# Optimization experiments

Hardware: AMD Instinct MI355X
Metric: run time of the kernel (lower is better)

Reference implementation:

```python
import jax, jax.numpy as jnp
import numpy as np

B, P, D = 32, 2048, 256  # batch, patch_num, input_dim


def setup_inputs() -> dict:
    key = jax.random.key(0)
    ks = jax.random.split(key, 6)
    n = lambda k, shape: jax.random.normal(k, shape, dtype=jnp.float32) * 0.02
    return {
        "x": jax.random.normal(ks[0], (B, P, D), dtype=jnp.float32),
        "mlp_w": n(ks[1], (D, D)), "mlp_b": jnp.zeros((D,), jnp.float32),
        "his_w": n(ks[2], (D, D)), "his_b": jnp.zeros((D,), jnp.float32),
        "cur_w": n(ks[3], (D, D)), "cur_b": jnp.zeros((D,), jnp.float32),
        "wl_w": n(ks[4], (D, P)), "wl_b": jnp.zeros((P,), jnp.float32),
        "gate_w": n(ks[5], (D, 1)), "gate_b": jnp.zeros((1,), jnp.float32),
        "ln_g": jnp.ones((D,), jnp.float32), "ln_b": jnp.zeros((D,), jnp.float32),
    }


def _layernorm(h, g, b, eps=1e-5):
    mu = h.mean(-1, keepdims=True)
    var = ((h - mu) ** 2).mean(-1, keepdims=True)
    return (h - mu) * jax.lax.rsqrt(var + eps) * g + b


def reference(x, mlp_w, mlp_b, his_w, his_b, cur_w, cur_b, wl_w, wl_b,
              gate_w, gate_b, ln_g, ln_b):
    origin = x
    # expert_num == 0 -> MoE branch skipped, x unchanged
    H = origin @ his_w + his_b                              # extractor_his: [B,P,D]
    # gate(extractor_cur(origin)) -> [B,P,1], repeated along last dim == broadcast
    weight_current = (origin @ cur_w + cur_b) @ gate_w + gate_b  # [B,P,1]
    logits = H @ wl_w + wl_b                                # [B,P,P]
    weight = jax.nn.softmax(logits, axis=-1)                # row softmax
    adj = jnp.tril(weight)                                  # causal mask (diagonal=0)
    aggregated = jnp.einsum('bpq,bqd->bpd', adj, origin)    # [B,P,D]
    H_history = aggregated @ mlp_w + mlp_b                  # dropout is identity (p=0)
    H_current = weight_current * origin
    out = _layernorm(H_history + H_current, ln_g, ln_b)     # aggregated_norm == 1
    return (out, origin)
```

## Files before the change

kernel.cpp:

```cpp
#include <hip/hip_runtime.h>
#include <hip/hip_bf16.h>

typedef __attribute__((ext_vector_type(8))) short s8v;
typedef __attribute__((ext_vector_type(4))) float f4v;
typedef __attribute__((ext_vector_type(4))) unsigned int u4v;

#define BATCH 32
#define SEQ   2048
#define DIM   256
#define ORIGIN_OFF ((size_t)BATCH * SEQ * DIM)

#define XT_OFF  0ull
#define WL_OFF  16777216ull
#define HIS_OFF 17301504ull
#define MLP_OFF 17367040ull

#define OFF_A 0
#define OFF_B 33792
#define OFF_C 79872
#define XT_LDS 9216

__device__ __forceinline__ unsigned short f2bf(float f) {
  __hip_bfloat16 h = __float2bfloat16(f);
  return *reinterpret_cast<unsigned short*>(&h);
}
__device__ __forceinline__ f4v mfma16(s8v a, s8v b, f4v c) {
  return __builtin_amdgcn_mfma_f32_16x16x32_bf16(a, b, c, 0, 0, 0);
}
__device__ __forceinline__ unsigned int pk2(float lo, float hi) {
  return (unsigned int)f2bf(lo) | ((unsigned int)f2bf(hi) << 16);
}
__device__ __forceinline__ void dma16(const void* g, void* l) {
  __builtin_amdgcn_global_load_lds(
      (const __attribute__((address_space(1))) unsigned int*)g,
      (__attribute__((address_space(3))) unsigned int*)l, 16, 0, 0);
}


__global__ __launch_bounds__(256) void prep_w(
    const float* __restrict__ wl_w, const float* __restrict__ his_w,
    const float* __restrict__ mlp_w, unsigned short* __restrict__ ws)
{
  const int gid = blockIdx.x * 256 + threadIdx.x;
  const int row = gid >> 5;
  const int c0 = (gid & 31) * 8;
  const float* src; unsigned short* dst; int ld;
  if (row < 2048)      { src = wl_w + row;           ld = 2048; dst = ws + WL_OFF  + (size_t)row * 256 + c0; }
  else if (row < 2304) { src = his_w + (row - 2048); ld = 256;  dst = ws + HIS_OFF + (size_t)(row - 2048) * 256 + c0; }
  else                 { src = mlp_w + (row - 2304); ld = 256;  dst = ws + MLP_OFF + (size_t)(row - 2304) * 256 + c0; }
  u4v o;
  #pragma unroll
  for (int j = 0; j < 4; ++j) {
    const unsigned short lo = f2bf(src[(size_t)(c0 + 2 * j) * ld]);
    const unsigned short hi = f2bf(src[(size_t)(c0 + 2 * j + 1) * ld]);
    o[j] = (unsigned int)lo | ((unsigned int)hi << 16);
  }
  *(u4v*)dst = o;
}

__global__ __launch_bounds__(256) void prep_xt(
    const float* __restrict__ x, unsigned short* __restrict__ xT)
{
  __shared__ unsigned short tile[64][68];
  const int b = blockIdx.z, p0 = blockIdx.x * 64, d0 = blockIdx.y * 64;
  const int t = threadIdx.x;
  {
    const int r = t >> 2, c0 = (t & 3) * 16;
    const float* src = x + ((size_t)b * SEQ + p0 + r) * DIM + d0 + c0;
    #pragma unroll
    for (int j = 0; j < 4; ++j) {
      f4v v = *(const f4v*)(src + j * 4);
      tile[r][c0 + j * 4 + 0] = f2bf(v[0]);
      tile[r][c0 + j * 4 + 1] = f2bf(v[1]);
      tile[r][c0 + j * 4 + 2] = f2bf(v[2]);
      tile[r][c0 + j * 4 + 3] = f2bf(v[3]);
    }
  }
  __syncthreads();
  {
    const int dl = t >> 2, s0 = (t & 3) * 16;
    u4v o0, o1;
    #pragma unroll
    for (int j = 0; j < 4; ++j) {
      o0[j] = (unsigned int)tile[s0 + 2 * j][dl]     | ((unsigned int)tile[s0 + 2 * j + 1][dl] << 16);
      o1[j] = (unsigned int)tile[s0 + 8 + 2 * j][dl] | ((unsigned int)tile[s0 + 9 + 2 * j][dl] << 16);
    }
    unsigned short* dst = xT + ((size_t)b * DIM + d0 + dl) * SEQ + p0 + s0;
    *(u4v*)dst = o0;
    *(u4v*)(dst + 8) = o1;
  }
}


__device__ __forceinline__ void gemm_regA(
    const unsigned short* __restrict__ Wt,
    const s8v (&af)[2][8], f4v (&acc)[2][8],
    char* smem_, int tid, int col16, int quad, int wc, int x7, int wq)
{
  char* sB = smem_ + OFF_B;
  char* ldsW = sB + wq * 1024;
  const int wrow = tid >> 5;
  const int wu = (tid & 31) ^ wrow;
  for (int st = 0; st < 4; ++st) {
    if (st) __syncthreads();
    const unsigned short* src = Wt + (size_t)(st * 64 + wrow) * 256 + wu * 8;
    #pragma unroll
    for (int j = 0; j < 8; ++j) dma16(src + (size_t)j * 2048, ldsW + j * 4096);
    __syncthreads();
    #pragma unroll
    for (int s = 0; s < 8; ++s) {
      const int sl = (((s * 4 + quad) ^ x7) << 4);
      #pragma unroll
      for (int nt = 0; nt < 2; ++nt) {
        s8v bfr = *(const s8v*)(sB + (wc * 32 + nt * 16 + col16) * 512 + sl);
        acc[0][st * 2 + nt] = mfma16(af[0][s], bfr, acc[0][st * 2 + nt]);
        acc[1][st * 2 + nt] = mfma16(af[1][s], bfr, acc[1][st * 2 + nt]);
      }
    }
  }
}

__global__ __launch_bounds__(256, 2)
void tfs_kernel(
    const float* __restrict__ x,
    const float* __restrict__ mlp_b,
    const float* __restrict__ his_b,
    const float* __restrict__ cur_w,
    const float* __restrict__ cur_b,
    const float* __restrict__ wl_b,
    const float* __restrict__ gate_w,
    const float* __restrict__ gate_b,
    const float* __restrict__ ln_g,
    const float* __restrict__ ln_b,
    const unsigned short* __restrict__ wsp,
    float* __restrict__ out)
{
  __shared__ __align__(16) char smem[81408];
  char* sA = smem + OFF_A;
  char* sB = smem + OFF_B;
  char* sC = smem + OFF_C;

  const int tid = threadIdx.x;
  const int lane = tid & 63;
  const int col16 = lane & 15;
  const int quad = lane >> 4;
  const int w = tid >> 6;
  const int wr = w & 1, wc = w >> 1;
  const int rw = wr * 32;
  const int x7 = col16 & 7;
  const int wq = __builtin_amdgcn_readfirstlane(w);

  const int b = blockIdx.y;
  const int pidx = (blockIdx.x + ((blockIdx.y >> 3) & 3) * 8) & 31;
  const int p0 = pidx * 64;

  const float* xb = x + (size_t)b * SEQ * DIM;
  const unsigned short* wlT  = wsp + WL_OFF;
  const unsigned short* hisT = wsp + HIS_OFF;
  const unsigned short* mlpT = wsp + MLP_OFF;
  const unsigned short* xTb  = wsp + XT_OFF + (size_t)b * DIM * SEQ;
  const f4v zero4 = {0.f, 0.f, 0.f, 0.f};

  const int krow = tid >> 5;
  const int ku   = (tid & 31) ^ krow;
  const int xrow = tid >> 3;
  const int xu   = (tid & 7) ^ (xrow & 7);
  char* ldsK = smem + OFF_A + wq * 1024;
  char* ldsX = smem + OFF_B + XT_LDS + wq * 1024;

  s8v xf[2][8];
  #pragma unroll
  for (int a = 0; a < 2; ++a) {
    const int row = rw + a * 16 + col16;
    const float* srcx = xb + (size_t)(p0 + row) * DIM;
    #pragma unroll
    for (int s = 0; s < 8; ++s) {
      const int k0 = (s * 4 + quad) * 8;
      f4v v0 = *(const f4v*)(srcx + k0);
      f4v v1 = *(const f4v*)(srcx + k0 + 4);
      u4v o;
      o[0] = pk2(v0[0], v0[1]); o[1] = pk2(v0[2], v0[3]);
      o[2] = pk2(v1[0], v1[1]); o[3] = pk2(v1[2], v1[3]);
      xf[a][s] = *(s8v*)&o;
    }
  }

  f4v accQ[2][8];
  #pragma unroll
  for (int a = 0; a < 2; ++a)
    #pragma unroll
    for (int i = 0; i < 8; ++i) accQ[a][i] = zero4;
  gemm_regA(hisT, xf, accQ, smem, tid, col16, quad, wc, x7, wq);
  #pragma unroll
  for (int a = 0; a < 2; ++a)
    #pragma unroll
    for (int i = 0; i < 8; ++i) {
      const int n = (i >> 1) * 64 + wc * 32 + (i & 1) * 16 + col16;
      const float bias = his_b[n];
      #pragma unroll
      for (int r = 0; r < 4; ++r) {
        const int row = rw + a * 16 + quad * 4 + r;
        *(unsigned short*)(sA + row * 528 + n * 2) = f2bf(accQ[a][i][r] + bias);
      }
    }
  __syncthreads();
  s8v qf[2][8];
  #pragma unroll
  for (int a = 0; a < 2; ++a) {
    const int row = rw + a * 16 + col16;
    #pragma unroll
    for (int s = 0; s < 8; ++s)
      qf[a][s] = *(const s8v*)(sA + row * 528 + (s * 4 + quad) * 16);
  }
  __syncthreads();
  {
    const unsigned short* srck = wlT + (size_t)krow * 256 + ku * 8;
    #pragma unroll
    for (int j = 0; j < 8; ++j) dma16(srck + (size_t)j * 2048, ldsK + j * 4096);
  }
  __syncthreads();

  f4v accO[2][8];
  #pragma unroll
  for (int a = 0; a < 2; ++a)
    #pragma unroll
    for (int dt = 0; dt < 8; ++dt) accO[a][dt] = zero4;
  float mrun[2][4], Zrun[2][4], mrunT[2];
  #pragma unroll
  for (int a = 0; a < 2; ++a) {
    mrunT[a] = -1.0e30f;
    #pragma unroll
    for (int r = 0; r < 4; ++r) { mrun[a][r] = -1.0e30f; Zrun[a][r] = 0.f; }
  }
  float* stat_max = (float*)(sC);
  float* stat_sum = (float*)(sC + 512);
  char* sX = sB + XT_LDS;
  const int rk0 = (wc * 32 + col16) * 512;
  const int rk1 = rk0 + 16 * 512;

  #pragma unroll 1
  for (int qi = 0; qi < 32; ++qi) {
    const int q0 = qi * 64;
    const bool active = (q0 <= p0);

    f4v accST[2][2];
    accST[0][0] = zero4; accST[0][1] = zero4;
    accST[1][0] = zero4; accST[1][1] = zero4;
    #pragma unroll
    for (int s = 0; s < 8; ++s) {
      const int sl = (((s * 4 + quad) ^ x7) << 4);
      s8v kf0 = *(const s8v*)(sA + rk0 + sl);
      s8v kf1 = *(const s8v*)(sA + rk1 + sl);
      accST[0][0] = mfma16(kf0, qf[0][s], accST[0][0]);
      accST[0][1] = mfma16(kf0, qf[1][s], accST[0][1]);
      accST[1][0] = mfma16(kf1, qf[0][s], accST[1][0]);
      accST[1][1] = mfma16(kf1, qf[1][s], accST[1][1]);
    }
    #pragma unroll
    for (int t = 0; t < 2; ++t) {
      const f4v wb = *(const f4v*)(wl_b + q0 + wc * 32 + t * 16 + quad * 4);
      #pragma unroll
      for (int a = 0; a < 2; ++a)
        #pragma unroll
        for (int r = 0; r < 4; ++r) accST[t][a][r] += wb[r];
    }
    #pragma unroll
    for (int a = 0; a < 2; ++a) {
      float m = fmaxf(fmaxf(fmaxf(accST[0][a][0], accST[0][a][1]),
                            fmaxf(accST[0][a][2], accST[0][a][3])),
                      fmaxf(fmaxf(accST[1][a][0], accST[1][a][1]),
                            fmaxf(accST[1][a][2], accST[1][a][3])));
      m = fmaxf(m, __shfl_xor(m, 16, 64));
      m = fmaxf(m, __shfl_xor(m, 32, 64));
      if (quad == 0) stat_max[wc * 64 + rw + a * 16 + col16] = m;
    }
    __syncthreads();

    if (qi < 31) {
      const unsigned short* srck = wlT + (size_t)(q0 + 64 + krow) * 256 + ku * 8;
      #pragma unroll
      for (int j = 0; j < 8; ++j) dma16(srck + (size_t)j * 2048, ldsK + j * 4096);
    }
    if (active) {
      const unsigned short* srcx = xTb + (size_t)xrow * 2048 + q0 + xu * 8;
      #pragma unroll
      for (int j = 0; j < 8; ++j) dma16(srcx + (size_t)j * 65536, ldsX + j * 4096);
    }

    float alpha[2][4];
    #pragma unroll
    for (int a = 0; a < 2; ++a)
      #pragma unroll
      for (int r = 0; r < 4; ++r) {
        const int row = rw + a * 16 + quad * 4 + r;
        const float mt = fmaxf(stat_max[row], stat_max[64 + row]);
        const float mn = fmaxf(mrun[a][r], mt);
        alpha[a][r] = __expf(fminf(mrun[a][r] - mn, 0.f));
        mrun[a][r] = mn;
      }
    #pragma unroll
    for (int a = 0; a < 2; ++a) {
      const int p = rw + a * 16 + col16;
      mrunT[a] = fmaxf(mrunT[a], fmaxf(stat_max[p], stat_max[64 + p]));
    }
    float Pv[2][2][4];
    #pragma unroll
    for (int t = 0; t < 2; ++t)
      #pragma unroll
      for (int a = 0; a < 2; ++a)
        #pragma unroll
        for (int r = 0; r < 4; ++r)
          Pv[t][a][r] = __expf(fminf(accST[t][a][r] - mrunT[a], 0.f));
    #pragma unroll
    for (int a = 0; a < 2; ++a) {
      float s = ((Pv[0][a][0] + Pv[0][a][1]) + (Pv[0][a][2] + Pv[0][a][3]))
              + ((Pv[1][a][0] + Pv[1][a][1]) + (Pv[1][a][2] + Pv[1][a][3]));
      s += __shfl_xor(s, 16, 64);
      s += __shfl_xor(s, 32, 64);
      if (quad == 0) stat_sum[wc * 64 + rw + a * 16 + col16] = s;
    }
    if (active) {
      #pragma unroll
      for (int t = 0; t < 2; ++t)
        #pragma unroll
        for (int a = 0; a < 2; ++a) {
          const int p = rw + a * 16 + col16;
          #pragma unroll
          for (int r = 0; r < 4; ++r) {
            const int ql = wc * 32 + t * 16 + quad * 4 + r;
            const float pv = ((q0 + ql) <= (p0 + p)) ? Pv[t][a][r] : 0.f;
            *(unsigned short*)(sB + p * 144 + ql * 2) = f2bf(pv);
          }
        }
    }
    __syncthreads();

    #pragma unroll
    for (int a = 0; a < 2; ++a)
      #pragma unroll
      for (int r = 0; r < 4; ++r) {
        const int row = rw + a * 16 + quad * 4 + r;
        const float st = stat_sum[row] + stat_sum[64 + row];
        Zrun[a][r] = Zrun[a][r] * alpha[a][r] + st;
      }
    #pragma unroll
    for (int a = 0; a < 2; ++a)
      #pragma unroll
      for (int dt = 0; dt < 8; ++dt)
        #pragma unroll
        for (int r = 0; r < 4; ++r) accO[a][dt][r] *= alpha[a][r];

    if (active) {
      #pragma unroll
      for (int h = 0; h < 2; ++h) {
        s8v ap0 = *(const s8v*)(sB + (rw + col16) * 144 + (h * 4 + quad) * 16);
        s8v ap1 = *(const s8v*)(sB + (rw + 16 + col16) * 144 + (h * 4 + quad) * 16);
        const int slx = (((h * 4 + quad) ^ x7) << 4);
        #pragma unroll
        for (int dt = 0; dt < 8; ++dt) {
          const int d = wc * 128 + dt * 16 + col16;
          s8v bv = *(const s8v*)(sX + d * 128 + slx);
          accO[0][dt] = mfma16(ap0, bv, accO[0][dt]);
          accO[1][dt] = mfma16(ap1, bv, accO[1][dt]);
        }
      }
    }
  }

  #pragma unroll
  for (int a = 0; a < 2; ++a)
    #pragma unroll
    for (int dt = 0; dt < 8; ++dt) {
      const int d = wc * 128 + dt * 16 + col16;
      #pragma unroll
      for (int r = 0; r < 4; ++r) {
        const int row = rw + a * 16 + quad * 4 + r;
        const float invZ = 1.0f / fmaxf(Zrun[a][r], 1e-30f);
        *(unsigned short*)(sA + row * 528 + d * 2) = f2bf(accO[a][dt][r] * invZ);
      }
    }
  __syncthreads();
  s8v af[2][8];
  #pragma unroll
  for (int a = 0; a < 2; ++a) {
    const int row = rw + a * 16 + col16;
    #pragma unroll
    for (int s = 0; s < 8; ++s)
      af[a][s] = *(const s8v*)(sA + row * 528 + (s * 4 + quad) * 16);
  }
  f4v accH[2][8];
  #pragma unroll
  for (int a = 0; a < 2; ++a)
    #pragma unroll
    for (int i = 0; i < 8; ++i) accH[a][i] = zero4;
  gemm_regA(mlpT, af, accH, smem, tid, col16, quad, wc, x7, wq);
  __syncthreads();

  float* cgL = (float*)(sB + 24576);
  float* cbL = (float*)(sB + 25600);
  {
    const float* cw = cur_w + (size_t)tid * DIM;
    float s = 0.f;
    #pragma unroll 8
    for (int i = 0; i < 64; ++i) {
      f4v vc = *(const f4v*)(cw + i * 4);
      f4v vg = *(const f4v*)(gate_w + i * 4);
      s += vc[0] * vg[0] + vc[1] * vg[1] + vc[2] * vg[2] + vc[3] * vg[3];
    }
    cgL[tid] = s;
    if (tid == 0) {
      float s2 = 0.f;
      for (int j = 0; j < DIM; ++j) s2 += cur_b[j] * gate_w[j];
      cbL[0] = s2 + gate_b[0];
    }
  }
  __syncthreads();

  float* wp = (float*)sC;
  {
    const int row = tid & 63, sg = tid >> 6;
    const float* xr = xb + (size_t)(p0 + row) * DIM + sg * 64;
    const float* cgp = cgL + sg * 64;
    float sacc = 0.f;
    #pragma unroll
    for (int i = 0; i < 16; ++i) {
      f4v xv4 = *(const f4v*)(xr + i * 4);
      sacc += xv4[0] * cgp[i * 4] + xv4[1] * cgp[i * 4 + 1]
            + xv4[2] * cgp[i * 4 + 2] + xv4[3] * cgp[i * 4 + 3];
    }
    wp[row * 4 + sg] = sacc;
  }
  __syncthreads();
  float* wcS = (float*)sC;
  if (tid < 64) {
    const float v = wp[tid * 4] + wp[tid * 4 + 1] + wp[tid * 4 + 2] + wp[tid * 4 + 3] + cbL[0];
    wcS[tid] = v;
  }
  __syncthreads();

  float s1l[2][4], s2l[2][4];
  #pragma unroll
  for (int a = 0; a < 2; ++a)
    #pragma unroll
    for (int r = 0; r < 4; ++r) { s1l[a][r] = 0.f; s2l[a][r] = 0.f; }
  #pragma unroll
  for (int a = 0; a < 2; ++a)
    #pragma unroll
    for (int i = 0; i < 8; ++i) {
      const int n = (i >> 1) * 64 + wc * 32 + (i & 1) * 16 + col16;
      const float mb = mlp_b[n];
      #pragma unroll
      for (int r = 0; r < 4; ++r) {
        const int row = rw + a * 16 + quad * 4 + r;
        const float xv = xb[(size_t)(p0 + row) * DIM + n];
        const float v = accH[a][i][r] + mb + wcS[row] * xv;
        accH[a][i][r] = v;
        s1l[a][r] += v;
        s2l[a][r] += v * v;
      }
    }
  #pragma unroll
  for (int a = 0; a < 2; ++a)
    #pragma unroll
    for (int r = 0; r < 4; ++r) {
      float v1 = s1l[a][r], v2 = s2l[a][r];
      v1 += __shfl_xor(v1, 1, 64); v2 += __shfl_xor(v2, 1, 64);
      v1 += __shfl_xor(v1, 2, 64); v2 += __shfl_xor(v2, 2, 64);
      v1 += __shfl_xor(v1, 4, 64); v2 += __shfl_xor(v2, 4, 64);
      v1 += __shfl_xor(v1, 8, 64); v2 += __shfl_xor(v2, 8, 64);
      s1l[a][r] = v1; s2l[a][r] = v2;
    }
  float* Ls = (float*)(sC + 256);
  float* Lq = (float*)(sC + 768);
  if (col16 == 0) {
    #pragma unroll
    for (int a = 0; a < 2; ++a)
      #pragma unroll
      for (int r = 0; r < 4; ++r) {
        const int row = rw + a * 16 + quad * 4 + r;
        Ls[wc * 64 + row] = s1l[a][r];
        Lq[wc * 64 + row] = s2l[a][r];
      }
  }
  __syncthreads();

  #pragma unroll
  for (int a = 0; a < 2; ++a) {
    float mean_[4], rstd_[4];
    #pragma unroll
    for (int r = 0; r < 4; ++r) {
      const int row = rw + a * 16 + quad * 4 + r;
      const float S1 = Ls[row] + Ls[64 + row];
      const float S2 = Lq[row] + Lq[64 + row];
      const float mean = S1 * (1.0f / 256.0f);
      const float var = S2 * (1.0f / 256.0f) - mean * mean;
      mean_[r] = mean;
      rstd_[r] = rsqrtf(fmaxf(var, 0.f) + 1e-5f);
    }
    #pragma unroll
    for (int i = 0; i < 8; ++i) {
      const int n = (i >> 1) * 64 + wc * 32 + (i & 1) * 16 + col16;
      const float g = ln_g[n];
      const float be = ln_b[n];
      #pragma unroll
      for (int r = 0; r < 4; ++r) {
        const int row = rw + a * 16 + quad * 4 + r;
        const float y = (accH[a][i][r] - mean_[r]) * rstd_[r] * g + be;
        out[((size_t)b * SEQ + p0 + row) * DIM + n] = y;
      }
    }
  }

  {
    const int row = tid >> 2, cs = (tid & 3) * 64;
    const float* src = xb + (size_t)(p0 + row) * DIM + cs;
    float* dst = out + ORIGIN_OFF + ((size_t)b * SEQ + p0 + row) * DIM + cs;
    #pragma unroll
    for (int j = 0; j < 16; ++j)
      *(f4v*)(dst + j * 4) = *(const f4v*)(src + j * 4);
  }
}

extern "C" void kernel_launch(void* const* d_in, const int* in_sizes, int n_in,
                              void* d_out, int out_size, void* d_ws, size_t ws_size,
                              hipStream_t stream) {
  const float* x      = (const float*)d_in[0];
  const float* mlp_w  = (const float*)d_in[1];
  const float* mlp_b  = (const float*)d_in[2];
  const float* his_w  = (const float*)d_in[3];
  const float* his_b  = (const float*)d_in[4];
  const float* cur_w  = (const float*)d_in[5];
  const float* cur_b  = (const float*)d_in[6];
  const float* wl_w   = (const float*)d_in[7];
  const float* wl_b   = (const float*)d_in[8];
  const float* gate_w = (const float*)d_in[9];
  const float* gate_b = (const float*)d_in[10];
  const float* ln_g   = (const float*)d_in[11];
  const float* ln_b   = (const float*)d_in[12];

  unsigned short* ws = (unsigned short*)d_ws;

  prep_w<<<dim3(320), 256, 0, stream>>>(wl_w, his_w, mlp_w, ws);
  prep_xt<<<dim3(32, 4, 32), 256, 0, stream>>>(x, ws + XT_OFF);
  tfs_kernel<<<dim3(32, 32), 256, 0, stream>>>(
      x, mlp_b, his_b, cur_w, cur_b, wl_b, gate_w, gate_b,
      ln_g, ln_b, ws, (float*)d_out);
}
```

Measured before the change: 494.2 us.

## Merge prep kernels, load xT and weights directly to registers, shrink LDS for occupancy

Folds the two prep kernels into one tiled transpose/convert kernel with swizzled LDS. In the main kernel, the LDS-staged weight GEMMs and the xT tile staging are replaced by direct global loads into registers. That cuts LDS from about 81KB to 46KB so launch bounds can rise to 3 blocks per CU. It also vectorises the P-tile stores and stat reads, skips the accumulator rescale when no row max changed, and reorders the block-to-tile mapping. The cost is more global/L2 traffic and higher register pressure, which could cause spills.

```diff
diff --git a/kernel.cpp b/kernel.cpp
--- a/kernel.cpp
+++ b/kernel.cpp
@@ -4,6 +4,7 @@
 typedef __attribute__((ext_vector_type(8))) short s8v;
 typedef __attribute__((ext_vector_type(4))) float f4v;
 typedef __attribute__((ext_vector_type(4))) unsigned int u4v;
+typedef __attribute__((ext_vector_type(2))) unsigned int u2v;
 
 #define BATCH 32
 #define SEQ   2048
@@ -15,10 +16,14 @@
 #define HIS_OFF 17301504ull
 #define MLP_OFF 17367040ull
 
-#define OFF_A 0
-#define OFF_B 33792
-#define OFF_C 79872
-#define XT_LDS 9216
+#define OFF_SP   33792
+#define OFF_SM   43008
+#define OFF_SS   43520
+#define EP_CG    43008
+#define EP_CB    44032
+#define EP_WP    44048
+#define EP_LS    45072
+#define EP_LQ    45584
 
 __device__ __forceinline__ unsigned short f2bf(float f) {
   __hip_bfloat16 h = __float2bfloat16(f);
@@ -36,91 +41,94 @@
       (__attribute__((address_space(3))) unsigned int*)l, 16, 0, 0);
 }
 
-
-__global__ __launch_bounds__(256) void prep_w(
-    const float* __restrict__ wl_w, const float* __restrict__ his_w,
-    const float* __restrict__ mlp_w, unsigned short* __restrict__ ws)
+__global__ __launch_bounds__(256) void prep_all(
+    const float* __restrict__ x, const float* __restrict__ wl_w,
+    const float* __restrict__ his_w, const float* __restrict__ mlp_w,
+    unsigned short* __restrict__ ws)
 {
-  const int gid = blockIdx.x * 256 + threadIdx.x;
-  const int row = gid >> 5;
-  const int c0 = (gid & 31) * 8;
-  const float* src; unsigned short* dst; int ld;
-  if (row < 2048)      { src = wl_w + row;           ld = 2048; dst = ws + WL_OFF  + (size_t)row * 256 + c0; }
-  else if (row < 2304) { src = his_w + (row - 2048); ld = 256;  dst = ws + HIS_OFF + (size_t)(row - 2048) * 256 + c0; }
-  else                 { src = mlp_w + (row - 2304); ld = 256;  dst = ws + MLP_OFF + (size_t)(row - 2304) * 256 + c0; }
-  u4v o;
-  #pragma unroll
-  for (int j = 0; j < 4; ++j) {
-    const unsigned short lo = f2bf(src[(size_t)(c0 + 2 * j) * ld]);
-    const unsigned short hi = f2bf(src[(size_t)(c0 + 2 * j + 1) * ld]);
-    o[j] = (unsigned int)lo | ((unsigned int)hi << 16);
-  }
-  *(u4v*)dst = o;
-}
-
-__global__ __launch_bounds__(256) void prep_xt(
-    const float* __restrict__ x, unsigned short* __restrict__ xT)
+  __shared__ unsigned short tile[64][72];
+  const int t = threadIdx.x;
+  const int tb = blockIdx.x;
+  const float* src; unsigned short* dst; int lds_, ldd_, r0, c0;
+  if (tb < 4096) {
+    const int b = tb >> 7, rem = tb & 127;
+    r0 = (rem >> 2) * 64;  c0 = (rem & 3) * 64;
+    src = x + (size_t)b * SEQ * DIM;  lds_ = DIM;
+    dst = ws + XT_OFF + (size_t)b * DIM * SEQ;  ldd_ = SEQ;
+  } else if (tb < 4224) {
+    const int t2 = tb - 4096;
+    r0 = (t2 >> 5) * 64;  c0 = (t2 & 31) * 64;
+    src = wl_w;  lds_ = 2048;  dst = ws + WL_OFF;  ldd_ = 256;
+  } else if (tb < 4240) {
+    const int t2 = tb - 4224;
+    r0 = (t2 >> 2) * 64;  c0 = (t2 & 3) * 64;
+    src = his_w;  lds_ = 256;  dst = ws + HIS_OFF;  ldd_ = 256;
+  } else {
+    const int t2 = tb - 4240;
+    r0 = (t2 >> 2) * 64;  c0 = (t2 & 3) * 64;
+    src = mlp_w;  lds_ = 256;  dst = ws + MLP_OFF;  ldd_ = 256;
+  }
+  {
+    const int rr = t >> 2, cc = (t & 3) * 16;
+    const float* s0 = src + (size_t)(r0 + rr) * lds_ + c0 + cc;
+    f4v v0 = *(const f4v*)(s0);
+    f4v v1 = *(const f4v*)(s0 + 4);
+    f4v v2 = *(const f4v*)(s0 + 8);
+    f4v v3 = *(const f4v*)(s0 + 12);
+    u4v o0, o1;
+    o0[0] = pk2(v0[0], v0[1]); o0[1] = pk2(v0[2], v0[3]);
+    o0[2] = pk2(v1[0], v1[1]); o0[3] = pk2(v1[2], v1[3]);
+    o1[0] = pk2(v2[0], v2[1]); o1[1] = pk2(v2[2], v2[3]);
+    o1[2] = pk2(v3[0], v3[1]); o1[3] = pk2(v3[2], v3[3]);
+    const int swz = rr >> 4;
+    const int ch = cc >> 3;
+    unsigned short* trow = &tile[rr][0];
+    *(u4v*)(trow + ((ch ^ swz) << 3)) = o0;
+    *(u4v*)(trow + (((ch + 1) ^ swz) << 3)) = o1;
+  }
+  __syncthreads();
+  {
+    const int cl = t >> 2, sg = t & 3;
+    const int chb = ((cl >> 3) ^ sg) << 3;
+    const int el = cl & 7;
+    u4v o0, o1;
+    #pragma unroll
+    for (int j = 0; j < 4; ++j) {
+      const int rA = sg * 16 + 2 * j;
+      o0[j] = (unsigned int)tile[rA][chb + el]
+            | ((unsigned int)tile[rA + 1][chb + el] << 16);
+    }
+    #pragma unroll
+    for (int j = 0; j < 4; ++j) {
+      const int rA = sg * 16 + 8 + 2 * j;
+      o1[j] = (unsigned int)tile[rA][chb + el]
+            | ((unsigned int)tile[rA + 1][chb + el] << 16);
+    }
+    unsigned short* d0 = dst + (size_t)(c0 + cl) * ldd_ + r0 + sg * 16;
+    *(u4v*)d0 = o0;
+    *(u4v*)(d0 + 8) = o1;
+  }
+}
+
+
+__device__ __forceinline__ void gemm_direct(
+    const unsigned short* __restrict__ Wt,
+    const s8v (&af)[2][8], f4v (&acc)[2][8], int col16, int quad, int wc)
 {
-  __shared__ unsigned short tile[64][68];
-  const int b = blockIdx.z, p0 = blockIdx.x * 64, d0 = blockIdx.y * 64;
-  const int t = threadIdx.x;
-  {
-    const int r = t >> 2, c0 = (t & 3) * 16;
-    const float* src = x + ((size_t)b * SEQ + p0 + r) * DIM + d0 + c0;
-    #pragma unroll
-    for (int j = 0; j < 4; ++j) {
-      f4v v = *(const f4v*)(src + j * 4);
-      tile[r][c0 + j * 4 + 0] = f2bf(v[0]);
-      tile[r][c0 + j * 4 + 1] = f2bf(v[1]);
-      tile[r][c0 + j * 4 + 2] = f2bf(v[2]);
-      tile[r][c0 + j * 4 + 3] = f2bf(v[3]);
-    }
-  }
-  __syncthreads();
-  {
-    const int dl = t >> 2, s0 = (t & 3) * 16;
-    u4v o0, o1;
-    #pragma unroll
-    for (int j = 0; j < 4; ++j) {
-      o0[j] = (unsigned int)tile[s0 + 2 * j][dl]     | ((unsigned int)tile[s0 + 2 * j + 1][dl] << 16);
-      o1[j] = (unsigned int)tile[s0 + 8 + 2 * j][dl] | ((unsigned int)tile[s0 + 9 + 2 * j][dl] << 16);
-    }
-    unsigned short* dst = xT + ((size_t)b * DIM + d0 + dl) * SEQ + p0 + s0;
-    *(u4v*)dst = o0;
-    *(u4v*)(dst + 8) = o1;
-  }
-}
-
-
-__device__ __forceinline__ void gemm_regA(
-    const unsigned short* __restrict__ Wt,
-    const s8v (&af)[2][8], f4v (&acc)[2][8],
-    char* smem_, int tid, int col16, int quad, int wc, int x7, int wq)
-{
-  char* sB = smem_ + OFF_B;
-  char* ldsW = sB + wq * 1024;
-  const int wrow = tid >> 5;
-  const int wu = (tid & 31) ^ wrow;
-  for (int st = 0; st < 4; ++st) {
-    if (st) __syncthreads();
-    const unsigned short* src = Wt + (size_t)(st * 64 + wrow) * 256 + wu * 8;
-    #pragma unroll
-    for (int j = 0; j < 8; ++j) dma16(src + (size_t)j * 2048, ldsW + j * 4096);
-    __syncthreads();
+  #pragma unroll
+  for (int i = 0; i < 8; ++i) {
+    const int n = (i >> 1) * 64 + wc * 32 + (i & 1) * 16 + col16;
+    const unsigned short* bp = Wt + (size_t)n * 256 + quad * 8;
     #pragma unroll
     for (int s = 0; s < 8; ++s) {
-      const int sl = (((s * 4 + quad) ^ x7) << 4);
-      #pragma unroll
-      for (int nt = 0; nt < 2; ++nt) {
-        s8v bfr = *(const s8v*)(sB + (wc * 32 + nt * 16 + col16) * 512 + sl);
-        acc[0][st * 2 + nt] = mfma16(af[0][s], bfr, acc[0][st * 2 + nt]);
-        acc[1][st * 2 + nt] = mfma16(af[1][s], bfr, acc[1][st * 2 + nt]);
-      }
-    }
-  }
-}
-
-__global__ __launch_bounds__(256, 2)
+      s8v bfr = *(const s8v*)(bp + s * 32);
+      acc[0][i] = mfma16(af[0][s], bfr, acc[0][i]);
+      acc[1][i] = mfma16(af[1][s], bfr, acc[1][i]);
+    }
+  }
+}
+
+__global__ __launch_bounds__(256, 3)
 void tfs_kernel(
     const float* __restrict__ x,
     const float* __restrict__ mlp_b,
@@ -135,10 +143,7 @@
     const unsigned short* __restrict__ wsp,
     float* __restrict__ out)
 {
-  __shared__ __align__(16) char smem[81408];
-  char* sA = smem + OFF_A;
-  char* sB = smem + OFF_B;
-  char* sC = smem + OFF_C;
+  __shared__ __align__(16) char smem[46336];
 
   const int tid = threadIdx.x;
   const int lane = tid & 63;
@@ -151,7 +156,8 @@
   const int wq = __builtin_amdgcn_readfirstlane(w);
 
   const int b = blockIdx.y;
-  const int pidx = (blockIdx.x + ((blockIdx.y >> 3) & 3) * 8) & 31;
+  const int bx = blockIdx.x;
+  const int pidx = ((((bx & 3) << 3) | (bx >> 2)) + b) & 31;
   const int p0 = pidx * 64;
 
   const float* xb = x + (size_t)b * SEQ * DIM;
@@ -163,10 +169,10 @@
 
   const int krow = tid >> 5;
   const int ku   = (tid & 31) ^ krow;
-  const int xrow = tid >> 3;
-  const int xu   = (tid & 7) ^ (xrow & 7);
-  char* ldsK = smem + OFF_A + wq * 1024;
-  char* ldsX = smem + OFF_B + XT_LDS + wq * 1024;
+  char* ldsK = smem + wq * 1024;
+  char* sP = smem + OFF_SP;
+  float* stat_max = (float*)(smem + OFF_SM);
+  float* stat_sum = (float*)(smem + OFF_SS);
 
   s8v xf[2][8];
   #pragma unroll
@@ -190,7 +196,7 @@
   for (int a = 0; a < 2; ++a)
     #pragma unroll
     for (int i = 0; i < 8; ++i) accQ[a][i] = zero4;
-  gemm_regA(hisT, xf, accQ, smem, tid, col16, quad, wc, x7, wq);
+  gemm_direct(hisT, xf, accQ, col16, quad, wc);
   #pragma unroll
   for (int a = 0; a < 2; ++a)
     #pragma unroll
@@ -200,7 +206,7 @@
       #pragma unroll
       for (int r = 0; r < 4; ++r) {
         const int row = rw + a * 16 + quad * 4 + r;
-        *(unsigned short*)(sA + row * 528 + n * 2) = f2bf(accQ[a][i][r] + bias);
+        *(unsigned short*)(smem + row * 528 + n * 2) = f2bf(accQ[a][i][r] + bias);
       }
     }
   __syncthreads();
@@ -210,7 +216,7 @@
     const int row = rw + a * 16 + col16;
     #pragma unroll
     for (int s = 0; s < 8; ++s)
-      qf[a][s] = *(const s8v*)(sA + row * 528 + (s * 4 + quad) * 16);
+      qf[a][s] = *(const s8v*)(smem + row * 528 + (s * 4 + quad) * 16);
   }
   __syncthreads();
   {
@@ -232,9 +238,6 @@
     #pragma unroll
     for (int r = 0; r < 4; ++r) { mrun[a][r] = -1.0e30f; Zrun[a][r] = 0.f; }
   }
-  float* stat_max = (float*)(sC);
-  float* stat_sum = (float*)(sC + 512);
-  char* sX = sB + XT_LDS;
   const int rk0 = (wc * 32 + col16) * 512;
   const int rk1 = rk0 + 16 * 512;
 
@@ -249,8 +252,8 @@
     #pragma unroll
     for (int s = 0; s < 8; ++s) {
       const int sl = (((s * 4 + quad) ^ x7) << 4);
-      s8v kf0 = *(const s8v*)(sA + rk0 + sl);
-      s8v kf1 = *(const s8v*)(sA + rk1 + sl);
+      s8v kf0 = *(const s8v*)(smem + rk0 + sl);
+      s8v kf1 = *(const s8v*)(smem + rk1 + sl);
       accST[0][0] = mfma16(kf0, qf[0][s], accST[0][0]);
       accST[0][1] = mfma16(kf0, qf[1][s], accST[0][1]);
       accST[1][0] = mfma16(kf1, qf[0][s], accST[1][0]);
@@ -281,23 +284,32 @@
       #pragma unroll
       for (int j = 0; j < 8; ++j) dma16(srck + (size_t)j * 2048, ldsK + j * 4096);
     }
+    s8v bv[2][8];
     if (active) {
-      const unsigned short* srcx = xTb + (size_t)xrow * 2048 + q0 + xu * 8;
-      #pragma unroll
-      for (int j = 0; j < 8; ++j) dma16(srcx + (size_t)j * 65536, ldsX + j * 4096);
+      #pragma unroll
+      for (int h = 0; h < 2; ++h)
+        #pragma unroll
+        for (int dt = 0; dt < 8; ++dt) {
+          const int d = wc * 128 + dt * 16 + col16;
+          bv[h][dt] = *(const s8v*)(xTb + (size_t)d * 2048 + q0 + (h * 4 + quad) * 8);
+        }
     }
 
     float alpha[2][4];
-    #pragma unroll
-    for (int a = 0; a < 2; ++a)
+    int anyr = 0;
+    #pragma unroll
+    for (int a = 0; a < 2; ++a) {
+      const f4v mlo = *(const f4v*)(stat_max + rw + a * 16 + quad * 4);
+      const f4v mhi = *(const f4v*)(stat_max + 64 + rw + a * 16 + quad * 4);
       #pragma unroll
       for (int r = 0; r < 4; ++r) {
-        const int row = rw + a * 16 + quad * 4 + r;
-        const float mt = fmaxf(stat_max[row], stat_max[64 + row]);
+        const float mt = fmaxf(mlo[r], mhi[r]);
         const float mn = fmaxf(mrun[a][r], mt);
+        anyr |= (mt > mrun[a][r]) ? 1 : 0;
         alpha[a][r] = __expf(fminf(mrun[a][r] - mn, 0.f));
         mrun[a][r] = mn;
       }
+    }
     #pragma unroll
     for (int a = 0; a < 2; ++a) {
       const int p = rw + a * 16 + col16;
@@ -325,43 +337,52 @@
         #pragma unroll
         for (int a = 0; a < 2; ++a) {
           const int p = rw + a * 16 + col16;
+          const int ql0 = wc * 32 + t * 16 + quad * 4;
+          const int lim = p0 + p - q0;
+          const float v0 = (ql0 + 0 <= lim) ? Pv[t][a][0] : 0.f;
+          const float v1 = (ql0 + 1 <= lim) ? Pv[t][a][1] : 0.f;
+          const float v2 = (ql0 + 2 <= lim) ? Pv[t][a][2] : 0.f;
+          const float v3 = (ql0 + 3 <= lim) ? Pv[t][a][3] : 0.f;
+          u2v pk; pk[0] = pk2(v0, v1); pk[1] = pk2(v2, v3);
+          *(u2v*)(sP + p * 144 + ql0 * 2) = pk;
+        }
+    }
+    __syncthreads();
+
+    if (__any(anyr)) {
+      #pragma unroll
+      for (int a = 0; a < 2; ++a) {
+        const f4v slo = *(const f4v*)(stat_sum + rw + a * 16 + quad * 4);
+        const f4v shi = *(const f4v*)(stat_sum + 64 + rw + a * 16 + quad * 4);
+        #pragma unroll
+        for (int r = 0; r < 4; ++r)
+          Zrun[a][r] = Zrun[a][r] * alpha[a][r] + (slo[r] + shi[r]);
+      }
+      #pragma unroll
+      for (int a = 0; a < 2; ++a)
+        #pragma unroll
+        for (int dt = 0; dt < 8; ++dt)
           #pragma unroll
-          for (int r = 0; r < 4; ++r) {
-            const int ql = wc * 32 + t * 16 + quad * 4 + r;
-            const float pv = ((q0 + ql) <= (p0 + p)) ? Pv[t][a][r] : 0.f;
-            *(unsigned short*)(sB + p * 144 + ql * 2) = f2bf(pv);
-          }
-        }
-    }
-    __syncthreads();
-
-    #pragma unroll
-    for (int a = 0; a < 2; ++a)
-      #pragma unroll
-      for (int r = 0; r < 4; ++r) {
-        const int row = rw + a * 16 + quad * 4 + r;
-        const float st = stat_sum[row] + stat_sum[64 + row];
-        Zrun[a][r] = Zrun[a][r] * alpha[a][r] + st;
-      }
-    #pragma unroll
-    for (int a = 0; a < 2; ++a)
-      #pragma unroll
-      for (int dt = 0; dt < 8; ++dt)
-        #pragma unroll
-        for (int r = 0; r < 4; ++r) accO[a][dt][r] *= alpha[a][r];
+          for (int r = 0; r < 4; ++r) accO[a][dt][r] *= alpha[a][r];
+    } else {
+      #pragma unroll
+      for (int a = 0; a < 2; ++a) {
+        const f4v slo = *(const f4v*)(stat_sum + rw + a * 16 + quad * 4);
+        const f4v shi = *(const f4v*)(stat_sum + 64 + rw + a * 16 + quad * 4);
+        #pragma unroll
+        for (int r = 0; r < 4; ++r) Zrun[a][r] += (slo[r] + shi[r]);
+      }
+    }
 
     if (active) {
       #pragma unroll
       for (int h = 0; h < 2; ++h) {
-        s8v ap0 = *(const s8v*)(sB + (rw + col16) * 144 + (h * 4 + quad) * 16);
-        s8v ap1 = *(const s8v*)(sB + (rw + 16 + col16) * 144 + (h * 4 + quad) * 16);
-        const int slx = (((h * 4 + quad) ^ x7) << 4);
+        s8v ap0 = *(const s8v*)(sP + (rw + col16) * 144 + (h * 4 + quad) * 16);
+        s8v ap1 = *(const s8v*)(sP + (rw + 16 + col16) * 144 + (h * 4 + quad) * 16);
         #pragma unroll
         for (int dt = 0; dt < 8; ++dt) {
-          const int d = wc * 128 + dt * 16 + col16;
-          s8v bv = *(const s8v*)(sX + d * 128 + slx);
-          accO[0][dt] = mfma16(ap0, bv, accO[0][dt]);
-          accO[1][dt] = mfma16(ap1, bv, accO[1][dt]);
+          accO[0][dt] = mfma16(ap0, bv[h][dt], accO[0][dt]);
+          accO[1][dt] = mfma16(ap1, bv[h][dt], accO[1][dt]);
         }
       }
     }
@@ -376,7 +397,7 @@
       for (int r = 0; r < 4; ++r) {
         const int row = rw + a * 16 + quad * 4 + r;
         const float invZ = 1.0f / fmaxf(Zrun[a][r], 1e-30f);
-        *(unsigned short*)(sA + row * 528 + d * 2) = f2bf(accO[a][dt][r] * invZ);
+        *(unsigned short*)(smem + row * 528 + d * 2) = f2bf(accO[a][dt][r] * invZ);
       }
     }
   __syncthreads();
@@ -386,18 +407,17 @@
     const int row = rw + a * 16 + col16;
     #pragma unroll
     for (int s = 0; s < 8; ++s)
-      af[a][s] = *(const s8v*)(sA + row * 528 + (s * 4 + quad) * 16);
+      af[a][s] = *(const s8v*)(smem + row * 528 + (s * 4 + quad) * 16);
   }
   f4v accH[2][8];
   #pragma unroll
   for (int a = 0; a < 2; ++a)
     #pragma unroll
     for (int i = 0; i < 8; ++i) accH[a][i] = zero4;
-  gemm_regA(mlpT, af, accH, smem, tid, col16, quad, wc, x7, wq);
-  __syncthreads();
-
-  float* cgL = (float*)(sB + 24576);
-  float* cbL = (float*)(sB + 25600);
+  gemm_direct(mlpT, af, accH, col16, quad, wc);
+
+  float* cgL = (float*)(smem + EP_CG);
+  float* cbL = (float*)(smem + EP_CB);
   {
     const float* cw = cur_w + (size_t)tid * DIM;
     float s = 0.f;
@@ -416,7 +436,7 @@
   }
   __syncthreads();
 
-  float* wp = (float*)sC;
+  float* wp = (float*)(smem + EP_WP);
   {
     const int row = tid & 63, sg = tid >> 6;
     const float* xr = xb + (size_t)(p0 + row) * DIM + sg * 64;
@@ -431,7 +451,7 @@
     wp[row * 4 + sg] = sacc;
   }
   __syncthreads();
-  float* wcS = (float*)sC;
+  float* wcS = (float*)(smem + EP_WP);
   if (tid < 64) {
     const float v = wp[tid * 4] + wp[tid * 4 + 1] + wp[tid * 4 + 2] + wp[tid * 4 + 3] + cbL[0];
     wcS[tid] = v;
@@ -470,8 +490,8 @@
       v1 += __shfl_xor(v1, 8, 64); v2 += __shfl_xor(v2, 8, 64);
       s1l[a][r] = v1; s2l[a][r] = v2;
     }
-  float* Ls = (float*)(sC + 256);
-  float* Lq = (float*)(sC + 768);
+  float* Ls = (float*)(smem + EP_LS);
+  float* Lq = (float*)(smem + EP_LQ);
   if (col16 == 0) {
     #pragma unroll
     for (int a = 0; a < 2; ++a)
@@ -540,8 +560,7 @@
 
   unsigned short* ws = (unsigned short*)d_ws;
 
-  prep_w<<<dim3(320), 256, 0, stream>>>(wl_w, his_w, mlp_w, ws);
-  prep_xt<<<dim3(32, 4, 32), 256, 0, stream>>>(x, ws + XT_OFF);
+  prep_all<<<dim3(4256), 256, 0, stream>>>(x, wl_w, his_w, mlp_w, ws);
   tfs_kernel<<<dim3(32, 32), 256, 0, stream>>>(
       x, mlp_b, his_b, cur_w, cur_b, wl_b, gate_w, gate_b,
       ln_g, ln_b, ws, (float*)d_out);
```

New measurement: 1.370 ms. +177.3%, slower.
